# Kernel optimization log

Hardware: AMD Instinct MI355X
Metric: run time of the kernel (lower is better)

Reference implementation:

```python
import jax, jax.numpy as jnp
import numpy as np

B, S, T = 4096, 512, 32


def setup_inputs() -> dict:
    key = jax.random.key(0)
    k1, k2, k3, k4, k5 = jax.random.split(key, 5)
    emissions = jax.random.normal(k1, (B, S, T), dtype=jnp.float32)
    tags = jax.random.randint(k2, (B, S), 0, T)
    mask = jnp.ones((B, S), dtype=bool)
    transitions = jax.random.normal(k3, (T, T), dtype=jnp.float32)
    start_transitions = jax.random.normal(k4, (T,), dtype=jnp.float32)
    end_transitions = jax.random.normal(k5, (T,), dtype=jnp.float32)
    return {
        "emissions": emissions,
        "tags": tags,
        "mask": mask,
        "transitions": transitions,
        "start_transitions": start_transitions,
        "end_transitions": end_transitions,
    }


def _score_sentence(emissions, tags, mask, transitions, start_transitions, end_transitions):
    # gold path score, fully vectorized over batch and time
    t0 = tags[:, 0]
    score = start_transitions[t0]
    score = score + jnp.take_along_axis(emissions[:, 0], t0[:, None], axis=1)[:, 0]
    maskf = mask[:, 1:].astype(emissions.dtype)  # [B, S-1]
    trans_sc = transitions[tags[:, :-1], tags[:, 1:]]  # [B, S-1]
    emit_sc = jnp.take_along_axis(emissions[:, 1:], tags[:, 1:, None], axis=2)[..., 0]
    score = score + ((trans_sc + emit_sc) * maskf).sum(axis=1)
    last_idx = mask.sum(axis=1).astype(jnp.int32) - 1  # [B]
    last_tags = jnp.take_along_axis(tags, last_idx[:, None], axis=1)[:, 0]
    score = score + end_transitions[last_tags]
    return score  # [B]


def _forward_algorithm(emissions, mask, transitions, start_transitions, end_transitions):
    # log partition via lax.scan over time; state is [B, T]
    score0 = start_transitions + emissions[:, 0]  # [B, T]
    em_rest = jnp.swapaxes(emissions[:, 1:], 0, 1)  # [S-1, B, T]
    mk_rest = jnp.swapaxes(mask[:, 1:], 0, 1)  # [S-1, B]

    def step(score, xs):
        em_i, m_i = xs
        # score[b,prev] + transitions[prev,next] + em_i[b,next]
        next_score = jax.nn.logsumexp(
            score[:, :, None] + transitions[None, :, :] + em_i[:, None, :], axis=1
        )
        score = jnp.where(m_i[:, None], next_score, score)
        return score, None

    score, _ = jax.lax.scan(step, score0, (em_rest, mk_rest))
    return jax.nn.logsumexp(score + end_transitions, axis=1)  # [B]


def reference(emissions, tags, mask, transitions, start_transitions, end_transitions):
    gold = _score_sentence(emissions, tags, mask, transitions, start_transitions, end_transitions)
    fwd = _forward_algorithm(emissions, mask, transitions, start_transitions, end_transitions)
    return (fwd - gold).mean()
```

## Files before the change

### kernel.cpp

```cpp
#include <hip/hip_runtime.h>
#include <hip/hip_bf16.h>


#define L2E 1.4426950408889634f
#define LN2 0.6931471805599453f
#define PD  8

__global__ __launch_bounds__(256) void crf_kernel(
    const float* __restrict__ emissions,
    const int*   __restrict__ tags,
    const float* __restrict__ transitions,
    const float* __restrict__ start_t,
    const float* __restrict__ end_t,
    float* __restrict__ out)
{
    constexpr int S = 512, T = 32;

    __shared__ float trans_raw[T * T];
    __shared__ float u_lds[8][T];
    __shared__ float res_lds[8];

    const int tid   = threadIdx.x;
    const int lane  = tid & 63;
    const int t     = lane & 31;
    const int slot  = tid >> 5;
    const int hbase = lane & 32;
    const long b    = (long)blockIdx.x * 8 + slot;

    #pragma unroll
    for (int k = 0; k < 4; ++k)
        trans_raw[tid + 256 * k] = transitions[tid + 256 * k];
    __syncthreads();

    float vv[T];
    #pragma unroll
    for (int k = 0; k < T; ++k)
        vv[k] = __builtin_amdgcn_exp2f(transitions[k * T + t] * L2E);

    const float* em_base = emissions + b * (long)(S * T) + t;
    const int*   tg_base = tags + b * S;

    float em0      = em_base[0];
    int   tag_prev = tg_base[0];

    float em_buf[PD];
    int   tag_buf[PD];
    #pragma unroll
    for (int j = 0; j < PD; ++j) {
        em_buf[j]  = em_base[(long)(1 + j) * T];
        tag_buf[j] = tg_base[1 + j];
    }

    float startv  = start_t[t];
    float r       = (startv + em0) * L2E;
    float offs    = 0.0f;
    float bk_prev = 0.0f;
    float gold = __shfl(startv, hbase + tag_prev, 64)
               + __shfl(em0,    hbase + tag_prev, 64);

    auto step = [&](int i, int bi) {
        float em_cur  = em_buf[bi];
        int   tag_cur = tag_buf[bi];
        int ip = i + PD; ip = (ip < S) ? ip : (S - 1);
        em_buf[bi]  = em_base[(long)ip * T];
        tag_buf[bi] = tg_base[ip];

        float u = __builtin_amdgcn_exp2f(r);
        u_lds[slot][t] = u;
        __builtin_amdgcn_wave_barrier();
        const float4* up = reinterpret_cast<const float4*>(&u_lds[slot][0]);
        float s0 = 0.f, s1 = 0.f, s2 = 0.f, s3 = 0.f;
        float s4 = 0.f, s5 = 0.f, s6 = 0.f, s7 = 0.f;
        #pragma unroll
        for (int j = 0; j < 4; ++j) {
            float4 ua = up[2 * j];
            float4 ub = up[2 * j + 1];
            s0 = fmaf(ua.x, vv[8 * j + 0], s0);
            s1 = fmaf(ua.y, vv[8 * j + 1], s1);
            s2 = fmaf(ua.z, vv[8 * j + 2], s2);
            s3 = fmaf(ua.w, vv[8 * j + 3], s3);
            s4 = fmaf(ub.x, vv[8 * j + 4], s4);
            s5 = fmaf(ub.y, vv[8 * j + 5], s5);
            s6 = fmaf(ub.z, vv[8 * j + 6], s6);
            s7 = fmaf(ub.w, vv[8 * j + 7], s7);
        }
        __builtin_amdgcn_wave_barrier();
        float s = ((s0 + s1) + (s2 + s3)) + ((s4 + s5) + (s6 + s7));

        float r_raw = fmaf(em_cur, L2E, __builtin_amdgcn_logf(s));
        r     = r_raw - bk_prev;
        offs += bk_prev;
        bk_prev = __shfl(r, hbase, 64);

        gold += trans_raw[tag_prev * 32 + tag_cur]
              + __shfl(em_cur, hbase + tag_cur, 64);
        tag_prev = tag_cur;
    };

    for (int ii = 1; ii < 505; ii += 8) {
        #pragma unroll
        for (int j = 0; j < 8; ++j) step(ii + j, j);
    }
    #pragma unroll
    for (int j = 0; j < 7; ++j) step(505 + j, j);

    float endv = end_t[t];
    gold += __shfl(endv, hbase + tag_prev, 64);

    float x = r + endv * L2E;
    float m = x;
    #pragma unroll
    for (int d = 16; d >= 1; d >>= 1) m = fmaxf(m, __shfl_xor(m, d, 64));
    float e = __builtin_amdgcn_exp2f(x - m);
    #pragma unroll
    for (int d = 16; d >= 1; d >>= 1) e += __shfl_xor(e, d, 64);
    float fwd2 = offs + m + __builtin_amdgcn_logf(e);

    float resv = fwd2 * LN2 - gold;

    if (t == 0) res_lds[slot] = resv;
    __syncthreads();
    if (tid == 0) {
        float acc = 0.0f;
        #pragma unroll
        for (int k = 0; k < 8; ++k) acc += res_lds[k];
        atomicAdd(out, acc * (1.0f / 4096.0f));
    }
}

extern "C" void kernel_launch(void* const* d_in, const int* in_sizes, int n_in,
                              void* d_out, int out_size, void* d_ws, size_t ws_size,
                              hipStream_t stream) {
    const float* emissions   = (const float*)d_in[0];
    const int*   tags        = (const int*)d_in[1];
    const float* transitions = (const float*)d_in[3];
    const float* start_t     = (const float*)d_in[4];
    const float* end_t       = (const float*)d_in[5];
    float* out = (float*)d_out;

    hipMemsetAsync(out, 0, sizeof(float), stream);
    crf_kernel<<<512, 256, 0, stream>>>(emissions, tags, transitions,
                                        start_t, end_t, out);
}
```

Baseline: 449.9 us.

## Split CRF forward reduction across wave halves, one sequence per wave

Each wave now processes a single sequence, with the two 32-lane halves each summing 16 of the 32 previous-tag terms using packed two-wide FMAs and combining via a cross-half shuffle. Gold-path lookups and the rescale offset use scalar readlane/readfirstlane instead of shuffles, and the emission prefetch depth grows to 16 steps. The grid doubles to 1024 blocks of 4 sequences with a launch-bounds occupancy hint. This shortens the per-step dependency chain of the serial recurrence at the cost of twice as many waves and an extra shuffle per step.

```diff
diff --git a/kernel.cpp b/kernel.cpp
--- a/kernel.cpp
+++ b/kernel.cpp
@@ -4,9 +4,18 @@
 
 #define L2E 1.4426950408889634f
 #define LN2 0.6931471805599453f
-#define PD  8
+#define PD  16
 
-__global__ __launch_bounds__(256) void crf_kernel(
+typedef float v2f __attribute__((ext_vector_type(2)));
+
+__device__ __forceinline__ float readlane_f(float v, int slane) {
+    return __uint_as_float(__builtin_amdgcn_readlane(__float_as_uint(v), slane));
+}
+__device__ __forceinline__ float readfirst_f(float v) {
+    return __uint_as_float(__builtin_amdgcn_readfirstlane(__float_as_uint(v)));
+}
+
+__global__ __launch_bounds__(256, 4) void crf_kernel(
     const float* __restrict__ emissions,
     const int*   __restrict__ tags,
     const float* __restrict__ transitions,
@@ -17,31 +26,35 @@
     constexpr int S = 512, T = 32;
 
     __shared__ float trans_raw[T * T];
-    __shared__ float u_lds[8][T];
-    __shared__ float res_lds[8];
+    __shared__ __align__(16) float u_lds[4][T];
+    __shared__ float res_lds[4];
 
-    const int tid   = threadIdx.x;
-    const int lane  = tid & 63;
-    const int t     = lane & 31;
-    const int slot  = tid >> 5;
-    const int hbase = lane & 32;
-    const long b    = (long)blockIdx.x * 8 + slot;
+    const int tid  = threadIdx.x;
+    const int lane = tid & 63;
+    const int tcol = lane & 31;
+    const int half = lane >> 5;
+    const int wv   = tid >> 6;
+    const long b   = (long)blockIdx.x * 4 + wv;
 
     #pragma unroll
     for (int k = 0; k < 4; ++k)
         trans_raw[tid + 256 * k] = transitions[tid + 256 * k];
     __syncthreads();
 
-    float vv[T];
+    const int koff = half * 16;
+    v2f vv2[8];
     #pragma unroll
-    for (int k = 0; k < T; ++k)
-        vv[k] = __builtin_amdgcn_exp2f(transitions[k * T + t] * L2E);
+    for (int j = 0; j < 8; ++j) {
+        float a = __builtin_amdgcn_exp2f(transitions[(koff + 2 * j)     * T + tcol] * L2E);
+        float c = __builtin_amdgcn_exp2f(transitions[(koff + 2 * j + 1) * T + tcol] * L2E);
+        vv2[j] = (v2f){a, c};
+    }
 
-    const float* em_base = emissions + b * (long)(S * T) + t;
+    const float* em_base = emissions + b * (long)(S * T) + tcol;
     const int*   tg_base = tags + b * S;
 
-    float em0      = em_base[0];
-    int   tag_prev = tg_base[0];
+    float em0   = em_base[0];
+    int   sprev = __builtin_amdgcn_readfirstlane(tg_base[0]);
 
     float em_buf[PD];
     int   tag_buf[PD];
@@ -51,61 +64,76 @@
         tag_buf[j] = tg_base[1 + j];
     }
 
-    float startv  = start_t[t];
+    float startv  = start_t[tcol];
     float r       = (startv + em0) * L2E;
     float offs    = 0.0f;
     float bk_prev = 0.0f;
-    float gold = __shfl(startv, hbase + tag_prev, 64)
-               + __shfl(em0,    hbase + tag_prev, 64);
+    float gold = readlane_f(startv, sprev) + readlane_f(em0, sprev);
 
-    auto step = [&](int i, int bi) {
-        float em_cur  = em_buf[bi];
-        int   tag_cur = tag_buf[bi];
-        int ip = i + PD; ip = (ip < S) ? ip : (S - 1);
-        em_buf[bi]  = em_base[(long)ip * T];
-        tag_buf[bi] = tg_base[ip];
+    float* u_row = &u_lds[wv][0];
+    const float4* up = reinterpret_cast<const float4*>(u_row + koff);
 
+    auto step = [&](float em_cur, int tag_cur) {
         float u = __builtin_amdgcn_exp2f(r);
-        u_lds[slot][t] = u;
+        u_row[tcol] = u;
         __builtin_amdgcn_wave_barrier();
-        const float4* up = reinterpret_cast<const float4*>(&u_lds[slot][0]);
-        float s0 = 0.f, s1 = 0.f, s2 = 0.f, s3 = 0.f;
-        float s4 = 0.f, s5 = 0.f, s6 = 0.f, s7 = 0.f;
-        #pragma unroll
-        for (int j = 0; j < 4; ++j) {
-            float4 ua = up[2 * j];
-            float4 ub = up[2 * j + 1];
-            s0 = fmaf(ua.x, vv[8 * j + 0], s0);
-            s1 = fmaf(ua.y, vv[8 * j + 1], s1);
-            s2 = fmaf(ua.z, vv[8 * j + 2], s2);
-            s3 = fmaf(ua.w, vv[8 * j + 3], s3);
-            s4 = fmaf(ub.x, vv[8 * j + 4], s4);
-            s5 = fmaf(ub.y, vv[8 * j + 5], s5);
-            s6 = fmaf(ub.z, vv[8 * j + 6], s6);
-            s7 = fmaf(ub.w, vv[8 * j + 7], s7);
-        }
+        float4 u0 = up[0], u1 = up[1], u2 = up[2], u3 = up[3];
         __builtin_amdgcn_wave_barrier();
-        float s = ((s0 + s1) + (s2 + s3)) + ((s4 + s5) + (s6 + s7));
+
+        v2f p0 = (v2f){u0.x, u0.y} * vv2[0];
+        p0 = __builtin_elementwise_fma((v2f){u0.z, u0.w}, vv2[1], p0);
+        v2f p1 = (v2f){u1.x, u1.y} * vv2[2];
+        p1 = __builtin_elementwise_fma((v2f){u1.z, u1.w}, vv2[3], p1);
+        v2f p2 = (v2f){u2.x, u2.y} * vv2[4];
+        p2 = __builtin_elementwise_fma((v2f){u2.z, u2.w}, vv2[5], p2);
+        v2f p3 = (v2f){u3.x, u3.y} * vv2[6];
+        p3 = __builtin_elementwise_fma((v2f){u3.z, u3.w}, vv2[7], p3);
+        v2f q = (p0 + p1) + (p2 + p3);
+        float s_half = q.x + q.y;
+        float s = s_half + __shfl_xor(s_half, 32, 64);
 
         float r_raw = fmaf(em_cur, L2E, __builtin_amdgcn_logf(s));
         r     = r_raw - bk_prev;
         offs += bk_prev;
-        bk_prev = __shfl(r, hbase, 64);
+        bk_prev = readfirst_f(r);
 
-        gold += trans_raw[tag_prev * 32 + tag_cur]
-              + __shfl(em_cur, hbase + tag_cur, 64);
-        tag_prev = tag_cur;
+        int scur = __builtin_amdgcn_readfirstlane(tag_cur);
+        gold += trans_raw[sprev * 32 + scur] + readlane_f(em_cur, scur);
+        sprev = scur;
     };
 
-    for (int ii = 1; ii < 505; ii += 8) {
+    for (int ii = 1; ii <= 465; ii += 16) {
+        const float* pf_em = em_base + (long)(ii + 16) * T;
+        const int*   pf_tg = tg_base + (ii + 16);
         #pragma unroll
-        for (int j = 0; j < 8; ++j) step(ii + j, j);
+        for (int j = 0; j < 16; ++j) {
+            float em_cur = em_buf[j];
+            int   tag_cur = tag_buf[j];
+            em_buf[j]  = pf_em[(long)j * T];
+            tag_buf[j] = pf_tg[j];
+            step(em_cur, tag_cur);
+        }
+    }
+    {
+        const float* pf_em = em_base + (long)497 * T;
+        const int*   pf_tg = tg_base + 497;
+        #pragma unroll
+        for (int j = 0; j < 15; ++j) {
+            float em_cur = em_buf[j];
+            int   tag_cur = tag_buf[j];
+            em_buf[j]  = pf_em[(long)j * T];
+            tag_buf[j] = pf_tg[j];
+            step(em_cur, tag_cur);
+        }
     }
     #pragma unroll
-    for (int j = 0; j < 7; ++j) step(505 + j, j);
+    for (int j = 0; j < 16; ++j) {
+        const int bi = (j + 15) & 15;
+        step(em_buf[bi], tag_buf[bi]);
+    }
 
-    float endv = end_t[t];
-    gold += __shfl(endv, hbase + tag_prev, 64);
+    float endv = end_t[tcol];
+    gold += readlane_f(endv, sprev);
 
     float x = r + endv * L2E;
     float m = x;
@@ -118,13 +146,11 @@
 
     float resv = fwd2 * LN2 - gold;
 
-    if (t == 0) res_lds[slot] = resv;
+    if (lane == 0) res_lds[wv] = resv;
     __syncthreads();
     if (tid == 0) {
-        float acc = 0.0f;
-        #pragma unroll
-        for (int k = 0; k < 8; ++k) acc += res_lds[k];
-        atomicAdd(out, acc * (1.0f / 4096.0f));
+        atomicAdd(out, (res_lds[0] + res_lds[1] + res_lds[2] + res_lds[3])
+                       * (1.0f / 4096.0f));
     }
 }
 
@@ -139,6 +165,6 @@
     float* out = (float*)d_out;
 
     hipMemsetAsync(out, 0, sizeof(float), stream);
-    crf_kernel<<<512, 256, 0, stream>>>(emissions, tags, transitions,
-                                        start_t, end_t, out);
+    crf_kernel<<<1024, 256, 0, stream>>>(emissions, tags, transitions,
+                                         start_t, end_t, out);
 }
```

Result: faster. 414.7 us (-7.8%).
